# Kernel tuning notes

Hardware: AMD Instinct MI355X
Metric: run time of the kernel (lower is better)

## Reference

```python
import jax, jax.numpy as jnp
import numpy as np

B, T, I = 32, 128, 512
H, L, O = 512, 2, 512


def _uniform(key, shape, std):
    return jax.random.uniform(key, shape, jnp.float32, -std, std)


def setup_inputs() -> dict:
    key = jax.random.key(0)
    ks = jax.random.split(key, 12)
    std = 1.0 / np.sqrt(H)
    inp = {
        "x": jax.random.normal(ks[0], (B, T, I), jnp.float32),
        # stacked params: [L, 2, ...]; dir 0 = forward cells, dir 1 = reverse cells
        "Wxh": _uniform(ks[1], (L, 2, I, 2 * H), std),
        "bxh": _uniform(ks[2], (L, 2, 2 * H), std),
        "Whh": _uniform(ks[3], (L, 2, H, 2 * H), std),
        "bhh": _uniform(ks[4], (L, 2, 2 * H), std),
        "Wxr": _uniform(ks[5], (L, 2, I, H), std),
        "bxr": _uniform(ks[6], (L, 2, H), std),
        "Whr": _uniform(ks[7], (L, 2, H, H), std),
        "bhr": _uniform(ks[8], (L, 2, H, ), std),
        "Wfc": _uniform(ks[9], (2 * H, O), 1.0 / np.sqrt(2 * H)),
        "bfc": _uniform(ks[10], (O,), 1.0 / np.sqrt(2 * H)),
    }
    return inp


def gru_layer(seq, Wxh_l, bxh_l, Whh_l, bhh_l, Wxr_l, bxr_l, Whr_l, bhr_l):
    # seq: [T, B, I]. Precompute input projections for all timesteps (one big GEMM),
    # then scan the sequential h-dependent part.
    xh = jnp.einsum('tbi,ih->tbh', seq, Wxh_l) + bxh_l  # [T,B,2H]
    xr = jnp.einsum('tbi,ih->tbh', seq, Wxr_l) + bxr_l  # [T,B,H]

    def step(h, inp):
        xh_t, xr_t = inp
        zr = xh_t + h @ Whh_l + bhh_l
        z, r = jnp.split(zr, 2, axis=-1)
        z = jax.nn.sigmoid(z)
        r = jax.nn.sigmoid(r)
        g = jnp.tanh((h @ Whr_l + bhr_l) * r + xr_t)
        h = z * h + (1.0 - z) * g
        return h, h

    h0 = jnp.zeros((seq.shape[1], Whh_l.shape[0]), seq.dtype)
    _, out = jax.lax.scan(step, h0, (xh, xr))
    return out  # [T,B,H]


def reference(x, Wxh, bxh, Whh, bhh, Wxr, bxr, Whr, bhr, Wfc, bfc):
    # Faithful translation of BidirRecurrentModel.forward (GRU mode):
    # forward stream scans time-ordered input; reverse stream independently scans
    # the time-reversed input (the two streams are NOT concatenated between layers).
    seq_f = jnp.transpose(x, (1, 0, 2))   # [T,B,I]
    seq_r = seq_f[::-1]                   # reversed time order
    n_layers = Wxh.shape[0]
    for l in range(n_layers):
        seq_f = gru_layer(seq_f, Wxh[l, 0], bxh[l, 0], Whh[l, 0], bhh[l, 0],
                          Wxr[l, 0], bxr[l, 0], Whr[l, 0], bhr[l, 0])
        seq_r = gru_layer(seq_r, Wxh[l, 1], bxh[l, 1], Whh[l, 1], bhh[l, 1],
                          Wxr[l, 1], bxr[l, 1], Whr[l, 1], bhr[l, 1])
    # out = last fwd timestep; out_rev = FIRST element of reverse-ordered stream
    # (i.e. the reverse cell's state after one step), exactly as in the source.
    out = jnp.concatenate([seq_f[-1], seq_r[0]], axis=1)  # [B, 2H]
    return out @ Wfc + bfc  # [B, O]
```

## Files before the change

kernel.cpp:

```cpp
#include <hip/hip_runtime.h>
#include <hip/hip_bf16.h>

#define PROJ_ELEMS 12582912
#define SEQ_ELEMS  4194304
#define SLAB_PER_BLK 6144

typedef float f32x4 __attribute__((ext_vector_type(4)));

__device__ unsigned g_slots[512];

__global__ __launch_bounds__(256)
void proj_kernel(const float* __restrict__ src,
                 const float* __restrict__ Wxh, const float* __restrict__ bxh,
                 const float* __restrict__ Wxr, const float* __restrict__ bxr,
                 __hip_bfloat16* __restrict__ proj, int layer)
{
    __shared__ float As[32][137];
    __shared__ float Ws[32][132];
    const int tid  = threadIdx.x;
    const int col0 = blockIdx.x * 128;
    const int row0 = blockIdx.y * 128;
    const int d    = row0 >> 12;
    const int ld   = layer * 2 + d;
    const int tx = tid & 15, ty = tid >> 4;

    const bool is_xr = (col0 >= 1024);
    const float* Wbase = is_xr ? (Wxr + (size_t)ld * 512 * 512 + (col0 - 1024))
                               : (Wxh + (size_t)ld * 512 * 1024 + col0);
    const int wstride = is_xr ? 512 : 1024;
    const float* bias = is_xr ? (bxr + ld * 512 + (col0 - 1024))
                              : (bxh + ld * 1024 + col0);

    float acc[8][8];
    #pragma unroll
    for (int i = 0; i < 8; i++)
        #pragma unroll
        for (int j = 0; j < 8; j++) acc[i][j] = 0.f;

    for (int k0 = 0; k0 < 512; k0 += 32) {
        #pragma unroll
        for (int v = 0; v < 4; v++) {
            int idx = tid + v * 256;
            int r   = idx >> 3;
            int c4  = (idx & 7) << 2;
            int gm  = row0 + r;
            int rr  = gm & 4095;
            int tt  = rr >> 5, bb = rr & 31;
            const float* p;
            if (layer == 0) {
                int ts = (gm >= 4096) ? (127 - tt) : tt;
                p = src + ((size_t)bb * 128 + ts) * 512 + (k0 + c4);
            } else {
                p = src + (((size_t)(gm >> 12) * 128 + tt) * 32 + bb) * 512 + (k0 + c4);
            }
            float4 vv = *(const float4*)p;
            As[c4 + 0][r] = vv.x; As[c4 + 1][r] = vv.y;
            As[c4 + 2][r] = vv.z; As[c4 + 3][r] = vv.w;
        }
        #pragma unroll
        for (int v = 0; v < 4; v++) {
            int idx = tid + v * 256;
            int kr  = idx >> 5;
            int c4  = (idx & 31) << 2;
            *(float4*)&Ws[kr][c4] = *(const float4*)(Wbase + (size_t)(k0 + kr) * wstride + c4);
        }
        __syncthreads();
        #pragma unroll
        for (int kk = 0; kk < 32; kk++) {
            float a[8], w[8];
            *(float4*)&a[0] = *(const float4*)&As[kk][ty * 8];
            *(float4*)&a[4] = *(const float4*)&As[kk][ty * 8 + 4];
            *(float4*)&w[0] = *(const float4*)&Ws[kk][tx * 8];
            *(float4*)&w[4] = *(const float4*)&Ws[kk][tx * 8 + 4];
            #pragma unroll
            for (int i = 0; i < 8; i++)
                #pragma unroll
                for (int j = 0; j < 8; j++)
                    acc[i][j] += a[i] * w[j];
        }
        __syncthreads();
    }
    #pragma unroll
    for (int i = 0; i < 8; i++) {
        int gm = row0 + ty * 8 + i;
        __hip_bfloat16* dst = proj + (size_t)gm * 1536 + col0 + tx * 8;
        #pragma unroll
        for (int j = 0; j < 8; j++)
            dst[j] = __float2bfloat16(acc[i][j] + bias[tx * 8 + j]);
    }
}

__global__ __launch_bounds__(256)
void repack_kernel(const float* __restrict__ Whh, const float* __restrict__ Whr,
                   float* __restrict__ slabs)
{
    if (blockIdx.x == 0) {
        g_slots[threadIdx.x] = 0u;
        g_slots[threadIdx.x + 256] = 0u;
    }
    const int blk = blockIdx.x;
    const int ld = blk >> 7, jb = blk & 127;
    const float* WhhL = Whh + (size_t)ld * 512 * 1024;
    const float* WhrL = Whr + (size_t)ld * 512 * 512;
    float* out = slabs + (size_t)blk * SLAB_PER_BLK;
    for (int u = 0; u < 24; u++) {
        int idx = threadIdx.x + u * 256;
        int rec = idx / 12, r3 = idx % 12;
        int g = rec >> 2, cg = rec & 3;
        int e = r3 >> 2, ki = r3 & 3;
        int k = g * 4 + ki, j = jb * 4 + cg;
        float v;
        if (e == 0)      v = WhhL[(size_t)k * 1024 + j];
        else if (e == 1) v = WhhL[(size_t)k * 1024 + 512 + j];
        else             v = WhrL[(size_t)k * 512 + j];
        out[idx] = v;
    }
}

__global__ __launch_bounds__(1024, 4)
void gru_seq_kernel(const __hip_bfloat16* __restrict__ proj, float* __restrict__ seq,
                    const float* __restrict__ slabs,
                    const float* __restrict__ bhh, const float* __restrict__ bhr,
                    int layer)
{
    __shared__ __align__(16) float hs[32 * 512];
    __shared__ __align__(16) float wlds[4100];
    const int tid = threadIdx.x;
    const int d   = blockIdx.x >> 7;
    const int jb  = blockIdx.x & 127;
    const int ld  = layer * 2 + d;
    const int cgi = tid & 3;
    const int kq  = (tid >> 2) & 7;
    const int b   = tid >> 5;
    const int j   = jb * 4 + cgi;
    const int sb  = b & 7;

    const f32x4* wrec = (const f32x4*)slabs + (size_t)(ld * 128 + jb) * 1536;
    const float bz = bhh[ld * 1024 + j];
    const float br = bhh[ld * 1024 + 512 + j];
    const float bg = bhr[ld * 512 + j];
    const float* hbase = seq + (size_t)(d * 128) * 32 * 512;
    const __hip_bfloat16* pbase = proj + ((size_t)(d * 128) * 32 + b) * 1536 + j;
    float* wout = seq + ((size_t)(d * 128) * 32 + b) * 512 + j;
    unsigned* slot_base = &g_slots[ld * 128];
    unsigned* myslot = slot_base + (tid & 127);

    {
        int i = tid;
        ((f32x4*)wlds)[i + (i >= 512 ? 1 : 0)] = wrec[(i >> 1) * 3 + (i & 1)];
    }

    __hip_bfloat16 rz = pbase[0], rr_ = pbase[512], rg = pbase[1024];

    for (int t = 0; t < 128; ++t) {
        if (t > 0) {
            const unsigned tgt = (unsigned)t;
            for (;;) {
                unsigned s = __hip_atomic_load(myslot, __ATOMIC_RELAXED,
                                               __HIP_MEMORY_SCOPE_AGENT);
                if (__all(s >= tgt)) break;
                __builtin_amdgcn_s_sleep(1);
            }
            const float* hsrc = hbase + (size_t)(t - 1) * 32 * 512;
            f32x4 tmp[4];
            #pragma unroll
            for (int v = 0; v < 4; v++) {
                int id = tid + v * 1024;
                asm volatile("global_load_dwordx4 %0, %1, off sc0 sc1"
                             : "=v"(tmp[v])
                             : "v"((const void*)(hsrc + (size_t)id * 4)));
            }
            asm volatile("s_waitcnt vmcnt(0)" ::: "memory");
            #pragma unroll
            for (int v = 0; v < 4; v++) {
                int id = tid + v * 1024;
                int bb = id >> 7, g = id & 127;
                int sl = g ^ (bb & 7) ^ ((g >> 4) & 7);
                *(f32x4*)&hs[bb * 512 + (sl << 2)] = tmp[v];
            }
        }
        __syncthreads();

        float pz = __bfloat162float(rz);
        float pr = __bfloat162float(rr_);
        float pg = __bfloat162float(rg);

        float az = 0.f, ar = 0.f, ag = 0.f;
        float hv_self = 0.f;
        if (t > 0) {
            #pragma unroll 4
            for (int gg = 0; gg < 16; gg++) {
                int g  = kq * 16 + gg;
                int sl = g ^ sb ^ kq;
                int rec = g * 4 + cgi;
                float4 h4 = *(const float4*)&hs[b * 512 + (sl << 2)];
                const f32x4* wp = (const f32x4*)wlds + (rec << 1) + (kq >> 2);
                f32x4 wz = wp[0], wr = wp[1];
                f32x4 wg = wrec[rec * 3 + 2];
                az += h4.x * wz.x + h4.y * wz.y + h4.z * wz.z + h4.w * wz.w;
                ar += h4.x * wr.x + h4.y * wr.y + h4.z * wr.z + h4.w * wr.w;
                ag += h4.x * wg.x + h4.y * wg.y + h4.z * wg.z + h4.w * wg.w;
            }
            az += __shfl_xor(az, 4, 64);  ar += __shfl_xor(ar, 4, 64);  ag += __shfl_xor(ag, 4, 64);
            az += __shfl_xor(az, 8, 64);  ar += __shfl_xor(ar, 8, 64);  ag += __shfl_xor(ag, 8, 64);
            az += __shfl_xor(az, 16, 64); ar += __shfl_xor(ar, 16, 64); ag += __shfl_xor(ag, 16, 64);
            hv_self = hs[b * 512 + ((jb ^ sb ^ (jb >> 4)) << 2) + cgi];
        }

        float z  = 1.f / (1.f + __expf(-(az + pz + bz)));
        float r  = 1.f / (1.f + __expf(-(ar + pr + br)));
        float gt = tanhf((ag + bg) * r + pg);
        float hn = z * hv_self + (1.f - z) * gt;
        if (kq == 0)
            __hip_atomic_store(wout + (size_t)t * 32 * 512, hn,
                               __ATOMIC_RELAXED, __HIP_MEMORY_SCOPE_AGENT);

        if (t < 127) {
            __syncthreads();
            if (tid == 0)
                __hip_atomic_store(slot_base + jb, (unsigned)(t + 1),
                                   __ATOMIC_RELAXED, __HIP_MEMORY_SCOPE_AGENT);
            const __hip_bfloat16* pn = pbase + (size_t)(t + 1) * 32 * 1536;
            rz = pn[0]; rr_ = pn[512]; rg = pn[1024];
        }
    }
}

__global__ __launch_bounds__(256)
void fc_kernel(const float* __restrict__ seq, const float* __restrict__ Wfc,
               const float* __restrict__ bfc, float* __restrict__ out)
{
    int idx = blockIdx.x * 256 + threadIdx.x;
    int b = idx >> 9, o = idx & 511;
    const float* catf = seq + ((size_t)(0 * 128 + 127) * 32 + b) * 512;
    const float* catr = seq + ((size_t)(1 * 128 + 0) * 32 + b) * 512;
    float acc = bfc[o];
    #pragma unroll 8
    for (int k = 0; k < 512; k++) acc += catf[k] * Wfc[(size_t)k * 512 + o];
    #pragma unroll 8
    for (int k = 0; k < 512; k++) acc += catr[k] * Wfc[(size_t)(512 + k) * 512 + o];
    out[(size_t)b * 512 + o] = acc;
}

extern "C" void kernel_launch(void* const* d_in, const int* in_sizes, int n_in,
                              void* d_out, int out_size, void* d_ws, size_t ws_size,
                              hipStream_t stream) {
    (void)in_sizes; (void)n_in; (void)out_size; (void)ws_size;
    const float* x   = (const float*)d_in[0];
    const float* Wxh = (const float*)d_in[1];
    const float* bxh = (const float*)d_in[2];
    const float* Whh = (const float*)d_in[3];
    const float* bhh = (const float*)d_in[4];
    const float* Wxr = (const float*)d_in[5];
    const float* bxr = (const float*)d_in[6];
    const float* Whr = (const float*)d_in[7];
    const float* bhr = (const float*)d_in[8];
    const float* Wfc = (const float*)d_in[9];
    const float* bfc = (const float*)d_in[10];
    float* out = (float*)d_out;

    char* base = (char*)d_ws;
    __hip_bfloat16* proj = (__hip_bfloat16*)base;
    float* seq   = (float*)(base + (size_t)PROJ_ELEMS * 2);
    float* slabs = seq + SEQ_ELEMS;

    repack_kernel<<<512, 256, 0, stream>>>(Whh, Whr, slabs);

    dim3 pgrid(12, 64);
    proj_kernel<<<pgrid, 256, 0, stream>>>(x, Wxh, bxh, Wxr, bxr, proj, 0);
    {
        int layer = 0;
        void* args[] = {(void*)&proj, (void*)&seq, (void*)&slabs,
                        (void*)&bhh, (void*)&bhr, (void*)&layer};
        hipLaunchCooperativeKernel((void*)gru_seq_kernel, dim3(256), dim3(1024),
                                   args, 0, stream);
    }
    proj_kernel<<<pgrid, 256, 0, stream>>>(seq, Wxh, bxh, Wxr, bxr, proj, 1);
    {
        int layer = 1;
        void* args[] = {(void*)&proj, (void*)&seq, (void*)&slabs,
                        (void*)&bhh, (void*)&bhr, (void*)&layer};
        hipLaunchCooperativeKernel((void*)gru_seq_kernel, dim3(256), dim3(1024),
                                   args, 0, stream);
    }
    fc_kernel<<<64, 256, 0, stream>>>(seq, Wfc, bfc, out);
}
```

Measured before the change: 2.617 ms.

## Read previous hidden state directly from global memory instead of staging in LDS

```diff
diff --git a/kernel.cpp b/kernel.cpp
--- a/kernel.cpp
+++ b/kernel.cpp
@@ -123,7 +123,6 @@
                     const float* __restrict__ bhh, const float* __restrict__ bhr,
                     int layer)
 {
-    __shared__ __align__(16) float hs[32 * 512];
     __shared__ __align__(16) float wlds[4100];
     const int tid = threadIdx.x;
     const int d   = blockIdx.x >> 7;
@@ -133,7 +132,6 @@
     const int kq  = (tid >> 2) & 7;
     const int b   = tid >> 5;
     const int j   = jb * 4 + cgi;
-    const int sb  = b & 7;
 
     const f32x4* wrec = (const f32x4*)slabs + (size_t)(ld * 128 + jb) * 1536;
     const float bz = bhh[ld * 1024 + j];
@@ -143,7 +141,8 @@
     const __hip_bfloat16* pbase = proj + ((size_t)(d * 128) * 32 + b) * 1536 + j;
     float* wout = seq + ((size_t)(d * 128) * 32 + b) * 512 + j;
     unsigned* slot_base = &g_slots[ld * 128];
-    unsigned* myslot = slot_base + (tid & 127);
+    unsigned* s0p = slot_base + (tid & 63);
+    unsigned* s1p = s0p + 64;
 
     {
         int i = tid;
@@ -151,49 +150,28 @@
     }
 
     __hip_bfloat16 rz = pbase[0], rr_ = pbase[512], rg = pbase[1024];
+    float hv_prev = 0.f;
 
     for (int t = 0; t < 128; ++t) {
+        float az = 0.f, ar = 0.f, ag = 0.f;
         if (t > 0) {
             const unsigned tgt = (unsigned)t;
             for (;;) {
-                unsigned s = __hip_atomic_load(myslot, __ATOMIC_RELAXED,
+                unsigned a = __hip_atomic_load(s0p, __ATOMIC_RELAXED,
                                                __HIP_MEMORY_SCOPE_AGENT);
-                if (__all(s >= tgt)) break;
+                unsigned c = __hip_atomic_load(s1p, __ATOMIC_RELAXED,
+                                               __HIP_MEMORY_SCOPE_AGENT);
+                if (__all(a >= tgt && c >= tgt)) break;
                 __builtin_amdgcn_s_sleep(1);
             }
-            const float* hsrc = hbase + (size_t)(t - 1) * 32 * 512;
-            f32x4 tmp[4];
-            #pragma unroll
-            for (int v = 0; v < 4; v++) {
-                int id = tid + v * 1024;
-                asm volatile("global_load_dwordx4 %0, %1, off sc0 sc1"
-                             : "=v"(tmp[v])
-                             : "v"((const void*)(hsrc + (size_t)id * 4)));
-            }
-            asm volatile("s_waitcnt vmcnt(0)" ::: "memory");
-            #pragma unroll
-            for (int v = 0; v < 4; v++) {
-                int id = tid + v * 1024;
-                int bb = id >> 7, g = id & 127;
-                int sl = g ^ (bb & 7) ^ ((g >> 4) & 7);
-                *(f32x4*)&hs[bb * 512 + (sl << 2)] = tmp[v];
-            }
-        }
-        __syncthreads();
-
-        float pz = __bfloat162float(rz);
-        float pr = __bfloat162float(rr_);
-        float pg = __bfloat162float(rg);
-
-        float az = 0.f, ar = 0.f, ag = 0.f;
-        float hv_self = 0.f;
-        if (t > 0) {
-            #pragma unroll 4
+            asm volatile("" ::: "memory");
+
+            const float* hrow = hbase + (size_t)(t - 1) * 32 * 512 + b * 512;
+            #pragma unroll 8
             for (int gg = 0; gg < 16; gg++) {
-                int g  = kq * 16 + gg;
-                int sl = g ^ sb ^ kq;
+                int g   = kq * 16 + gg;
                 int rec = g * 4 + cgi;
-                float4 h4 = *(const float4*)&hs[b * 512 + (sl << 2)];
+                float4 h4 = *(const float4*)(hrow + g * 4);
                 const f32x4* wp = (const f32x4*)wlds + (rec << 1) + (kq >> 2);
                 f32x4 wz = wp[0], wr = wp[1];
                 f32x4 wg = wrec[rec * 3 + 2];
@@ -204,13 +182,16 @@
             az += __shfl_xor(az, 4, 64);  ar += __shfl_xor(ar, 4, 64);  ag += __shfl_xor(ag, 4, 64);
             az += __shfl_xor(az, 8, 64);  ar += __shfl_xor(ar, 8, 64);  ag += __shfl_xor(ag, 8, 64);
             az += __shfl_xor(az, 16, 64); ar += __shfl_xor(ar, 16, 64); ag += __shfl_xor(ag, 16, 64);
-            hv_self = hs[b * 512 + ((jb ^ sb ^ (jb >> 4)) << 2) + cgi];
-        }
-
+        }
+
+        float pz = __bfloat162float(rz);
+        float pr = __bfloat162float(rr_);
+        float pg = __bfloat162float(rg);
         float z  = 1.f / (1.f + __expf(-(az + pz + bz)));
         float r  = 1.f / (1.f + __expf(-(ar + pr + br)));
         float gt = tanhf((ag + bg) * r + pg);
-        float hn = z * hv_self + (1.f - z) * gt;
+        float hn = z * hv_prev + (1.f - z) * gt;
+        hv_prev = hn;
         if (kq == 0)
             __hip_atomic_store(wout + (size_t)t * 32 * 512, hn,
                                __ATOMIC_RELAXED, __HIP_MEMORY_SCOPE_AGENT);
```

Result: slower. 3.104 ms (+18.6%).
